# Kernel optimization log

Hardware: AMD Instinct MI355X
Metric: run time of the kernel (lower is better)

The kernel has to match this reference:

```python
import jax, jax.numpy as jnp
import numpy as np

EPS = 1e-5

def _conv3x3(x, w):
    # x: [n,c,h,w], w: [o,c,3,3], stride 1, padding 1 (SAME)
    return jax.lax.conv_general_dilated(x, w, (1, 1), 'SAME',
                                        dimension_numbers=('NCHW', 'OIHW', 'NCHW'))

def _bn(x, g, b, m, v):
    # inference-mode BatchNorm2d with running stats
    s = g / jnp.sqrt(v + EPS)
    return x * s[:, None, None] + (b - m * s)[:, None, None]

def _lrelu(x):
    return jnp.where(x > 0, x, 0.2 * x)

def _conv1x1(x, w, b):
    # w: [o,c] (1x1 conv kernel collapsed)
    return jnp.einsum('nchw,oc->nohw', x, w) + b[:, None, None]

def _conv_relu(x, w, g, b, m, v):
    return _lrelu(_bn(_conv3x3(x, w), g, b, m, v))

def _pam(f, Wq, bq, Wk, bk, Wv, bv, alpha):
    n, c, h, w = f.shape
    hw = h * w
    q = _conv1x1(f, Wq, bq).reshape(n, -1, hw)   # [n,cr,hw]
    k = _conv1x1(f, Wk, bk).reshape(n, -1, hw)   # [n,cr,hw]
    # attention[i,j] over spatial tokens, softmax along j
    attn = jax.nn.softmax(jnp.einsum('nci,ncj->nij', q, k), axis=-1)  # [n,hw,hw]
    v = _conv1x1(f, Wv, bv).reshape(n, c, hw)    # [n,c,hw]
    # torch: bmm(v, attn^T) -> out[:, :, i] = sum_j v[:, :, j] * attn[i, j]
    out = jnp.einsum('ncj,nij->nci', v, attn).reshape(n, c, h, w)
    return alpha * out + f

def _cam(f, W1, b1, W2, b2):
    s = jnp.mean(f, axis=(2, 3), keepdims=True)  # AdaptiveAvgPool2d(1)
    s = _lrelu(_conv1x1(s, W1, b1))
    s = jax.nn.sigmoid(_conv1x1(s, W2, b2))
    return f * s

def _upx2(x):
    n, c, h, w = x.shape
    return jax.image.resize(x, (n, c, 2 * h, 2 * w), 'bilinear')

def setup_inputs() -> dict:
    key = jax.random.key(0)
    ks = jax.random.split(key, 16)
    N, C, H, W_ = 4, 512, 64, 64
    CR, NC = C // 8, 64
    f32 = jnp.float32
    def nrm(k, shape, s=0.05):
        return jax.random.normal(k, shape, f32) * s
    return {
        'x': jax.random.normal(ks[0], (N, C, H, W_), f32),
        'W_pam_in': nrm(ks[1], (C, C, 3, 3)),
        'pam_gamma': jnp.ones((C,), f32), 'pam_beta': jnp.zeros((C,), f32),
        'pam_mean': nrm(ks[2], (C,)), 'pam_var': jax.random.uniform(ks[3], (C,), f32) + 0.5,
        'Wq': nrm(ks[4], (CR, C)), 'bq': jnp.zeros((CR,), f32),
        'Wk': nrm(ks[5], (CR, C)), 'bk': jnp.zeros((CR,), f32),
        'Wv': nrm(ks[6], (C, C)), 'bv': jnp.zeros((C,), f32),
        'alpha': nrm(ks[7], (1,), 1.0),
        'W_pam_out': nrm(ks[8], (NC, C)), 'b_pam_out': jnp.zeros((NC,), f32),
        'W_cam_in': nrm(ks[9], (C, C, 3, 3)),
        'cam_gamma': jnp.ones((C,), f32), 'cam_beta': jnp.zeros((C,), f32),
        'cam_mean': nrm(ks[10], (C,)), 'cam_var': jax.random.uniform(ks[11], (C,), f32) + 0.5,
        'Wc1': nrm(ks[12], (CR, C)), 'bc1': jnp.zeros((CR,), f32),
        'Wc2': nrm(ks[13], (C, CR)), 'bc2': jnp.zeros((C,), f32),
        'W_cam_out': nrm(ks[14], (NC, C)), 'b_cam_out': jnp.zeros((NC,), f32),
    }

def reference(x, W_pam_in, pam_gamma, pam_beta, pam_mean, pam_var,
              Wq, bq, Wk, bk, Wv, bv, alpha, W_pam_out, b_pam_out,
              W_cam_in, cam_gamma, cam_beta, cam_mean, cam_var,
              Wc1, bc1, Wc2, bc2, W_cam_out, b_cam_out):
    pam_feat = _conv_relu(x, W_pam_in, pam_gamma, pam_beta, pam_mean, pam_var)
    pam_feat = _pam(pam_feat, Wq, bq, Wk, bk, Wv, bv, alpha)
    pam_feat = _upx2(_conv1x1(pam_feat, W_pam_out, b_pam_out))
    cam_feat = _conv_relu(x, W_cam_in, cam_gamma, cam_beta, cam_mean, cam_var)
    cam_feat = _cam(cam_feat, Wc1, bc1, Wc2, bc2)
    cam_feat = _upx2(_conv1x1(cam_feat, W_cam_out, b_cam_out))
    return pam_feat + cam_feat
```

## Files before the change

### kernel.cpp

```cpp
#include <hip/hip_runtime.h>
#include <hip/hip_bf16.h>
#include <math.h>

#define N_  4
#define C_  512
#define H_  64
#define W_  64
#define HW_ 4096
#define CR_ 64
#define NC_ 64
#define EPSV 1e-5f

typedef __attribute__((ext_vector_type(8))) __bf16 bf16x8;
typedef __attribute__((ext_vector_type(4))) float f32x4;
typedef __hip_bfloat16 bf16s;

__device__ __forceinline__ unsigned short bfb(float f) {
    union { bf16s h; unsigned short u; } cv;
    cv.h = __float2bfloat16(f);
    return cv.u;
}

__device__ __forceinline__ int swz8(int row, int ch) {
    return row * 64 + ((ch ^ (row & 7)) << 3);
}

__global__ __launch_bounds__(256) void k_xpose(
    const float* __restrict__ x, bf16s* __restrict__ xbT)
{
    __shared__ float xs[64][65];
    const int tid = threadIdx.x;
    const int n = blockIdx.z, c0 = blockIdx.y * 64, p0 = blockIdx.x * 64;
    for (int e = tid; e < 4096; e += 256) {
        int ci = e >> 6, pi = e & 63;
        xs[ci][pi] = x[((size_t)(n*C_ + c0 + ci))*HW_ + p0 + pi];
    }
    __syncthreads();
    for (int e = tid; e < 4096; e += 256) {
        int pi = e >> 6, ci = e & 63;
        xbT[((size_t)n*HW_ + p0 + pi)*C_ + c0 + ci] = __float2bfloat16(xs[ci][pi]);
    }
}

__global__ __launch_bounds__(256) void k_wprep(
    const float* __restrict__ w, bf16s* __restrict__ wb)
{
    int e = blockIdx.x * 256 + threadIdx.x;
    int c = e & 511; int r = e >> 9;
    int tap = r % 9; int o = r / 9;
    wb[e] = __float2bfloat16(w[((size_t)o*C_ + c)*9 + tap]);
}

__global__ __launch_bounds__(256) void k_wcast(
    const float* __restrict__ in, bf16s* __restrict__ out, int nElem)
{
    int e = blockIdx.x * 256 + threadIdx.x;
    if (e < nElem) out[e] = __float2bfloat16(in[e]);
}

__global__ __launch_bounds__(256, 2) void k_conv3x3_mfma(
    const bf16s* __restrict__ xbT, const bf16s* __restrict__ wb,
    const float* __restrict__ gamma, const float* __restrict__ beta,
    const float* __restrict__ mean, const float* __restrict__ var,
    float* __restrict__ out, bf16s* __restrict__ featT,
    float* __restrict__ csum, int mode)
{
    __shared__ bf16s aL[3][128][40];
    __shared__ bf16s bL[132][40];
    const int tid = threadIdx.x;
    const int n  = blockIdx.z;
    const int o0 = blockIdx.y * 128;
    const int pt = blockIdx.x;
    const int y0 = pt * 2;
    const int lane = tid & 63;
    const int wid  = tid >> 6;
    const int wr = wid >> 1, wc = wid & 1;
    const int lr = lane & 15, cb = lane >> 4;

    const int ao  = tid >> 2;
    const int ac  = (tid & 3) * 8;
    const int t0  = tid >> 2;
    const int t1  = t0 + 64;
    const int t2  = t0 + 128;
    const int ry1 = t1 >= 66 ? 1 : 0;
    const int xi1 = t1 - (ry1 ? 66 : 0);

    f32x4 acc[4][4];
#pragma unroll
    for (int i = 0; i < 4; ++i)
#pragma unroll
        for (int j = 0; j < 4; ++j) acc[i][j] = (f32x4){0.f,0.f,0.f,0.f};

    int4 pA0, pA1, pA2, pA3, pA4, pA5, pB0, pB1, pB2;

#define CONV_AADDR(DXI, OHALF, C0, DYI) \
    (const int4*)(wb + ((size_t)(o0 + (OHALF) + ao)*9 + (DYI)*3 + (DXI))*C_ + (C0) + ac)

#define CONV_BLOAD(DST, RY, XI, C0, DYI, VALID)                               \
    {                                                                         \
        int row_ = y0 + (DYI) - 1 + (RY);                                     \
        int xc_  = (XI) - 1;                                                  \
        int4 v_ = {0,0,0,0};                                                  \
        if ((VALID) && row_ >= 0 && row_ < H_ && xc_ >= 0 && xc_ < W_)        \
            v_ = *(const int4*)(xbT +                                         \
                ((size_t)n*HW_ + row_*W_ + xc_)*C_ + (C0) + ac);              \
        DST = v_;                                                             \
    }

#define CONV_ISSUE(C0, DYI)                                                   \
    {                                                                         \
        pA0 = *CONV_AADDR(0,  0, C0, DYI);                                    \
        pA1 = *CONV_AADDR(0, 64, C0, DYI);                                    \
        pA2 = *CONV_AADDR(1,  0, C0, DYI);                                    \
        pA3 = *CONV_AADDR(1, 64, C0, DYI);                                    \
        pA4 = *CONV_AADDR(2,  0, C0, DYI);                                    \
        pA5 = *CONV_AADDR(2, 64, C0, DYI);                                    \
        CONV_BLOAD(pB0, 0, t0, C0, DYI, 1)                                    \
        CONV_BLOAD(pB1, ry1, xi1, C0, DYI, 1)                                 \
        CONV_BLOAD(pB2, 1, t2 - 66, C0, DYI, tid < 16)                        \
    }

    CONV_ISSUE(0, 0)
    int c0 = 0, dyi = 0;
    for (int it = 0; it < 48; ++it) {
        *(int4*)&aL[0][ao][ac]      = pA0;
        *(int4*)&aL[0][64 + ao][ac] = pA1;
        *(int4*)&aL[1][ao][ac]      = pA2;
        *(int4*)&aL[1][64 + ao][ac] = pA3;
        *(int4*)&aL[2][ao][ac]      = pA4;
        *(int4*)&aL[2][64 + ao][ac] = pA5;
        *(int4*)&bL[t0][ac] = pB0;
        *(int4*)&bL[t1][ac] = pB1;
        if (tid < 16) *(int4*)&bL[t2][ac] = pB2;
        __syncthreads();
        int nd = dyi + 1, nc = c0;
        if (nd == 3) { nd = 0; nc += 32; }
        if (it < 47) CONV_ISSUE(nc, nd)
#pragma unroll
        for (int dxi = 0; dxi < 3; ++dxi) {
            bf16x8 af[4], bfv[4];
#pragma unroll
            for (int fm = 0; fm < 4; ++fm)
                af[fm] = *(const bf16x8*)&aL[dxi][wr*64 + fm*16 + lr][cb*8];
#pragma unroll
            for (int fn = 0; fn < 4; ++fn) {
                int pg = wc*64 + fn*16 + lr;
                int ry = pg >> 6, xc = pg & 63;
                bfv[fn] = *(const bf16x8*)&bL[ry*66 + xc + dxi][cb*8];
            }
#pragma unroll
            for (int fm = 0; fm < 4; ++fm)
#pragma unroll
                for (int fn = 0; fn < 4; ++fn)
                    acc[fm][fn] = __builtin_amdgcn_mfma_f32_16x16x32_bf16(
                        af[fm], bfv[fn], acc[fm][fn], 0, 0, 0);
        }
        __syncthreads();
        c0 = nc; dyi = nd;
    }
#undef CONV_ISSUE
#undef CONV_BLOAD
#undef CONV_AADDR
#pragma unroll
    for (int fm = 0; fm < 4; ++fm) {
        float sc[4], sh[4];
        const int obase = o0 + wr*64 + fm*16 + cb*4;
#pragma unroll
        for (int r = 0; r < 4; ++r) {
            int o = obase + r;
            sc[r] = gamma[o] * rsqrtf(var[o] + EPSV);
            sh[r] = beta[o] - mean[o]*sc[r];
        }
        float ps[4] = {0.f, 0.f, 0.f, 0.f};
#pragma unroll
        for (int fn = 0; fn < 4; ++fn) {
            int pg = wc*64 + fn*16 + lr;
            int p  = pt*128 + pg;
            float vv[4];
#pragma unroll
            for (int r = 0; r < 4; ++r) {
                float t = fmaf(acc[fm][fn][r], sc[r], sh[r]);
                vv[r] = t > 0.f ? t : 0.2f*t;
                if (mode == 0)
                    out[((size_t)(n*C_ + obase + r))*HW_ + p] = vv[r];
                else
                    ps[r] += vv[r];
            }
            uint2 u;
            u.x = (unsigned)bfb(vv[0]) | ((unsigned)bfb(vv[1]) << 16);
            u.y = (unsigned)bfb(vv[2]) | ((unsigned)bfb(vv[3]) << 16);
            *(uint2*)&featT[((size_t)n*HW_ + p)*C_ + obase] = u;
        }
        if (mode != 0) {
#pragma unroll
            for (int r = 0; r < 4; ++r) {
                float s = ps[r];
                s += __shfl_xor(s, 1);
                s += __shfl_xor(s, 2);
                s += __shfl_xor(s, 4);
                s += __shfl_xor(s, 8);
                if (lr == 0) atomicAdd(&csum[n*C_ + obase + r], s);
            }
        }
    }
}

__global__ __launch_bounds__(256, 2) void k_gemm(
    const bf16s* __restrict__ A, const bf16s* __restrict__ Bt,
    const float* __restrict__ bias, const float* __restrict__ scale,
    void* __restrict__ outp, int O, int mode)
{
    __shared__ bf16s aL[64][40];
    __shared__ bf16s bL[256][40];
    const int tid = threadIdx.x;
    const int n  = blockIdx.z;
    const int p0 = blockIdx.x * 256;
    const int o0 = blockIdx.y * 64;
    const int lane = tid & 63;
    const int wid  = tid >> 6;
    const int lr = lane & 15, cb = lane >> 4;
    const int arow = tid >> 2, ach = (tid & 3) * 8;

    f32x4 acc[4][4];
#pragma unroll
    for (int i = 0; i < 4; ++i)
#pragma unroll
        for (int j = 0; j < 4; ++j) acc[i][j] = (f32x4){0.f,0.f,0.f,0.f};

    int4 pA, pB0, pB1, pB2, pB3;
    float4 pS0, pS1;

#define GEMM_ISSUE(C0)                                                        \
    {                                                                         \
        pA = *(const int4*)&A[(size_t)(o0 + arow)*C_ + (C0) + ach];           \
        if (scale) {                                                          \
            pS0 = *(const float4*)&scale[(size_t)n*C_ + (C0) + ach];          \
            pS1 = *(const float4*)&scale[(size_t)n*C_ + (C0) + ach + 4];      \
        }                                                                     \
        pB0 = *(const int4*)&Bt[((size_t)n*HW_ + p0 + arow      )*C_ + (C0) + ach]; \
        pB1 = *(const int4*)&Bt[((size_t)n*HW_ + p0 + arow +  64)*C_ + (C0) + ach]; \
        pB2 = *(const int4*)&Bt[((size_t)n*HW_ + p0 + arow + 128)*C_ + (C0) + ach]; \
        pB3 = *(const int4*)&Bt[((size_t)n*HW_ + p0 + arow + 192)*C_ + (C0) + ach]; \
    }

    GEMM_ISSUE(0)
    for (int c0 = 0; c0 < C_; c0 += 32) {
        if (scale) {
            const bf16s* sp = (const bf16s*)&pA;
            bf16s tmp[8];
            tmp[0] = __float2bfloat16(__bfloat162float(sp[0]) * pS0.x);
            tmp[1] = __float2bfloat16(__bfloat162float(sp[1]) * pS0.y);
            tmp[2] = __float2bfloat16(__bfloat162float(sp[2]) * pS0.z);
            tmp[3] = __float2bfloat16(__bfloat162float(sp[3]) * pS0.w);
            tmp[4] = __float2bfloat16(__bfloat162float(sp[4]) * pS1.x);
            tmp[5] = __float2bfloat16(__bfloat162float(sp[5]) * pS1.y);
            tmp[6] = __float2bfloat16(__bfloat162float(sp[6]) * pS1.z);
            tmp[7] = __float2bfloat16(__bfloat162float(sp[7]) * pS1.w);
            *(int4*)&aL[arow][ach] = *(int4*)tmp;
        } else {
            *(int4*)&aL[arow][ach] = pA;
        }
        *(int4*)&bL[arow      ][ach] = pB0;
        *(int4*)&bL[arow +  64][ach] = pB1;
        *(int4*)&bL[arow + 128][ach] = pB2;
        *(int4*)&bL[arow + 192][ach] = pB3;
        __syncthreads();
        if (c0 + 32 < C_) GEMM_ISSUE(c0 + 32)
        bf16x8 af[4], bfv[4];
#pragma unroll
        for (int fo = 0; fo < 4; ++fo)
            af[fo] = *(const bf16x8*)&aL[fo*16 + lr][cb*8];
#pragma unroll
        for (int fp = 0; fp < 4; ++fp)
            bfv[fp] = *(const bf16x8*)&bL[wid*64 + fp*16 + lr][cb*8];
#pragma unroll
        for (int fo = 0; fo < 4; ++fo)
#pragma unroll
            for (int fp = 0; fp < 4; ++fp)
                acc[fo][fp] = __builtin_amdgcn_mfma_f32_16x16x32_bf16(
                    af[fo], bfv[fp], acc[fo][fp], 0, 0, 0);
        __syncthreads();
    }
#undef GEMM_ISSUE
#pragma unroll
    for (int fo = 0; fo < 4; ++fo) {
        const int obase = o0 + fo*16 + cb*4;
        float bv[4];
#pragma unroll
        for (int r = 0; r < 4; ++r) bv[r] = bias[obase + r];
#pragma unroll
        for (int fp = 0; fp < 4; ++fp) {
            int p = p0 + wid*64 + fp*16 + lr;
            float v[4];
#pragma unroll
            for (int r = 0; r < 4; ++r) v[r] = acc[fo][fp][r] + bv[r];
            if (mode == 1) {
                uint2 u;
                u.x = (unsigned)bfb(v[0]) | ((unsigned)bfb(v[1]) << 16);
                u.y = (unsigned)bfb(v[2]) | ((unsigned)bfb(v[3]) << 16);
                *(uint2*)&((bf16s*)outp)[((size_t)n*HW_ + p)*O + (obase - o0)] = u;
            } else if (mode == 2) {
#pragma unroll
                for (int r = 0; r < 4; ++r)
                    ((bf16s*)outp)[((size_t)(n*O + obase + r))*HW_ + p] =
                        __float2bfloat16(v[r]);
            } else {
#pragma unroll
                for (int r = 0; r < 4; ++r)
                    ((float*)outp)[((size_t)(n*O + obase + r))*HW_ + p] = v[r];
            }
        }
    }
}

__global__ __launch_bounds__(256) void k_rowstats_mfma(
    const bf16s* __restrict__ qb, const bf16s* __restrict__ kb,
    float* __restrict__ rowm, float* __restrict__ rowl)
{
    __shared__ bf16s qs[4096];
    __shared__ bf16s ks[4096];
    const int tid = threadIdx.x;
    const int lid = blockIdx.x + (blockIdx.y << 6) + (blockIdx.z << 8);
    const int n  = lid & 3;
    const int jz = (lid >> 2) & 1;
    const int i0 = (lid >> 3) << 6;
    const int lane = tid & 63;
    const int wid  = tid >> 6;
    const int lr = lane & 15, cb = lane >> 4;

    for (int e = tid; e < 512; e += 256) {
        int row = e >> 3, ch = e & 7;
        *(int4*)&qs[swz8(row, ch)] =
            *(const int4*)&qb[((size_t)n*HW_ + i0 + row)*CR_ + ch*8];
    }
    const int krow = tid >> 3, kch = tid & 7;
    const bf16s* kbase = kb + (size_t)n*HW_*CR_ + (size_t)jz*2048*CR_ + kch*8;
    int4 kreg0 = *(const int4*)(kbase + (size_t)krow*CR_);
    int4 kreg1 = *(const int4*)(kbase + (size_t)(krow + 32)*CR_);
    __syncthreads();
    bf16x8 bq[2];
#pragma unroll
    for (int kk = 0; kk < 2; ++kk)
        bq[kk] = *(const bf16x8*)&qs[swz8(wid*16 + lr, kk*4 + cb)];

    float m_t = -INFINITY, l_t = 0.f;
    for (int t = 0; t < 32; ++t) {
        __syncthreads();
        *(int4*)&ks[swz8(krow, kch)] = kreg0;
        *(int4*)&ks[swz8(krow + 32, kch)] = kreg1;
        if (t < 31) {
            kreg0 = *(const int4*)(kbase + (size_t)((t+1)*64 + krow)*CR_);
            kreg1 = *(const int4*)(kbase + (size_t)((t+1)*64 + krow + 32)*CR_);
        }
        __syncthreads();
        f32x4 sv[4];
#pragma unroll
        for (int fj = 0; fj < 4; ++fj) {
            f32x4 s = (f32x4){0.f,0.f,0.f,0.f};
#pragma unroll
            for (int kk = 0; kk < 2; ++kk) {
                bf16x8 ak = *(const bf16x8*)&ks[swz8(fj*16 + lr, kk*4 + cb)];
                s = __builtin_amdgcn_mfma_f32_16x16x32_bf16(ak, bq[kk], s, 0, 0, 0);
            }
            sv[fj] = s;
        }
        float mx = m_t;
#pragma unroll
        for (int fj = 0; fj < 4; ++fj)
#pragma unroll
            for (int r = 0; r < 4; ++r) mx = fmaxf(mx, sv[fj][r]);
        float sum = 0.f;
#pragma unroll
        for (int fj = 0; fj < 4; ++fj)
#pragma unroll
            for (int r = 0; r < 4; ++r) sum += __expf(sv[fj][r] - mx);
        l_t = l_t * __expf(m_t - mx) + sum;
        m_t = mx;
    }
#pragma unroll
    for (int mask = 16; mask <= 32; mask <<= 1) {
        float mo = __shfl_xor(m_t, mask);
        float lo = __shfl_xor(l_t, mask);
        float m2 = fmaxf(m_t, mo);
        l_t = l_t * __expf(m_t - m2) + lo * __expf(mo - m2);
        m_t = m2;
    }
    if (cb == 0) {
        rowm[((size_t)jz*N_ + n)*HW_ + i0 + wid*16 + lr] = m_t;
        rowl[((size_t)jz*N_ + n)*HW_ + i0 + wid*16 + lr] = l_t;
    }
}

__global__ __launch_bounds__(256, 4) void k_pv_mfma(
    const bf16s* __restrict__ qb, const bf16s* __restrict__ kb,
    const bf16s* __restrict__ vb, const float* __restrict__ rowm,
    const float* __restrict__ rowl, const float* __restrict__ alpha,
    const float* __restrict__ feat, bf16s* __restrict__ featT)
{
    __shared__ bf16s ks[4096];
    __shared__ bf16s qps[4096];
    const int tid = threadIdx.x;
    const int lid = blockIdx.x + (blockIdx.y << 6) + (blockIdx.z << 8);
    const int k8  = lid & 7;
    const int n   = k8 >> 1;
    const int cc0 = (((lid >> 3) & 1) * 2 + (k8 & 1)) << 7;
    const int i0  = (lid >> 4) << 6;
    const int lane = tid & 63;
    const int wid  = tid >> 6;
    const int lr = lane & 15, cb = lane >> 4;

    for (int e = tid; e < 512; e += 256) {
        int row = e >> 3, ch = e & 7;
        *(int4*)&qps[swz8(row, ch)] =
            *(const int4*)&qb[((size_t)n*HW_ + i0 + row)*CR_ + ch*8];
    }
    const int krow = tid >> 3, kch = tid & 7;
    const bf16s* kbase = kb + (size_t)n*HW_*CR_ + kch*8;
    int4 kreg0 = *(const int4*)(kbase + (size_t)krow*CR_);
    int4 kreg1 = *(const int4*)(kbase + (size_t)(krow + 32)*CR_);
    __syncthreads();
    bf16x8 bq[2];
#pragma unroll
    for (int kk = 0; kk < 2; ++kk)
        bq[kk] = *(const bf16x8*)&qps[swz8(wid*16 + lr, kk*4 + cb)];

    const size_t sidx = (size_t)n*HW_ + i0 + wid*16 + lr;
    const float m0 = rowm[sidx], m1 = rowm[sidx + (size_t)N_*HW_];
    const float l0 = rowl[sidx], l1 = rowl[sidx + (size_t)N_*HW_];
    const float mreg = fmaxf(m0, m1);
    const float rinv = 1.f / (l0*__expf(m0 - mreg) + l1*__expf(m1 - mreg));
    const float al = alpha[0];

    f32x4 acc[2][4];
#pragma unroll
    for (int i = 0; i < 2; ++i)
#pragma unroll
        for (int j = 0; j < 4; ++j) acc[i][j] = (f32x4){0.f,0.f,0.f,0.f};

    const bf16s* vbase = vb + ((size_t)(n*C_ + cc0 + wid*32))*HW_;

    for (int jt = 0; jt < 64; ++jt) {
        *(int4*)&ks[swz8(krow, kch)] = kreg0;
        *(int4*)&ks[swz8(krow + 32, kch)] = kreg1;
        if (jt < 63) {
            kreg0 = *(const int4*)(kbase + (size_t)((jt+1)*64 + krow)*CR_);
            kreg1 = *(const int4*)(kbase + (size_t)((jt+1)*64 + krow + 32)*CR_);
        }
        __syncthreads();
#pragma unroll
        for (int fj = 0; fj < 4; ++fj) {
            f32x4 s = (f32x4){0.f,0.f,0.f,0.f};
#pragma unroll
            for (int kk = 0; kk < 2; ++kk) {
                bf16x8 ak = *(const bf16x8*)&ks[swz8(fj*16 + lr, kk*4 + cb)];
                s = __builtin_amdgcn_mfma_f32_16x16x32_bf16(ak, bq[kk], s, 0, 0, 0);
            }
            unsigned short b[4];
#pragma unroll
            for (int r = 0; r < 4; ++r)
                b[r] = bfb(__expf(s[r] - mreg) * rinv);
            uint2 u;
            u.x = (unsigned)b[0] | ((unsigned)b[1] << 16);
            u.y = (unsigned)b[2] | ((unsigned)b[3] << 16);
            *(uint2*)&qps[swz8(wid*16 + lr, fj*2 + (cb >> 1)) + (cb & 1)*4] = u;
        }
        __syncthreads();
        const bf16s* vj = vbase + jt*64;
#pragma unroll
        for (int kk2 = 0; kk2 < 2; ++kk2) {
            bf16x8 vf[2], pa[4];
#pragma unroll
            for (int fc2 = 0; fc2 < 2; ++fc2)
                vf[fc2] = *(const bf16x8*)(vj + (size_t)(fc2*16 + lr)*HW_
                                              + kk2*32 + cb*8);
#pragma unroll
            for (int fi = 0; fi < 4; ++fi)
                pa[fi] = *(const bf16x8*)&qps[swz8(fi*16 + lr, kk2*4 + cb)];
#pragma unroll
            for (int fc2 = 0; fc2 < 2; ++fc2)
#pragma unroll
                for (int fi = 0; fi < 4; ++fi)
                    acc[fc2][fi] = __builtin_amdgcn_mfma_f32_16x16x32_bf16(
                        vf[fc2], pa[fi], acc[fc2][fi], 0, 0, 0);
        }
    }
#pragma unroll
    for (int fc2 = 0; fc2 < 2; ++fc2) {
        const int ccl = wid*32 + fc2*16 + cb*4;
#pragma unroll
        for (int fi = 0; fi < 4; ++fi) {
            const int p = i0 + fi*16 + lr;
            const float* fp = &feat[((size_t)(n*C_ + cc0 + ccl))*HW_ + p];
            float v0 = fmaf(al, acc[fc2][fi][0], fp[0]);
            float v1 = fmaf(al, acc[fc2][fi][1], fp[(size_t)HW_]);
            float v2 = fmaf(al, acc[fc2][fi][2], fp[(size_t)2*HW_]);
            float v3 = fmaf(al, acc[fc2][fi][3], fp[(size_t)3*HW_]);
            uint2 u;
            u.x = (unsigned)bfb(v0) | ((unsigned)bfb(v1) << 16);
            u.y = (unsigned)bfb(v2) | ((unsigned)bfb(v3) << 16);
            *(uint2*)&featT[((size_t)n*HW_ + p)*C_ + cc0 + ccl] = u;
        }
    }
}

__global__ __launch_bounds__(64) void k_cmlp(
    const float* __restrict__ s0, const float* __restrict__ Wc1,
    const float* __restrict__ bc1, const float* __restrict__ Wc2,
    const float* __restrict__ bc2, float* __restrict__ s2)
{
    const int n = blockIdx.x, tid = threadIdx.x;
    __shared__ float s1s[64];
    float a = 0.f;
    for (int c = 0; c < C_; ++c)
        a = fmaf(Wc1[(size_t)tid*C_ + c], s0[n*C_ + c] * (1.f/HW_), a);
    a += bc1[tid];
    a = a > 0.f ? a : 0.2f*a;
    s1s[tid] = a;
    __syncthreads();
    for (int c = tid; c < C_; c += 64) {
        float b = 0.f;
        for (int i = 0; i < CR_; ++i) b = fmaf(Wc2[(size_t)c*CR_ + i], s1s[i], b);
        b += bc2[c];
        s2[n*C_ + c] = 1.f / (1.f + __expf(-b));
    }
}

__global__ __launch_bounds__(256) void k_up(
    const float* __restrict__ pl, const float* __restrict__ cl,
    float* __restrict__ out)
{
    int idx = blockIdx.x * 256 + threadIdx.x;
    int ox = idx & 127; int rest = idx >> 7;
    int oy = rest & 127; rest >>= 7;
    int o  = rest & 63;  int n = rest >> 6;
    float fy = oy*0.5f - 0.25f;
    float fx = ox*0.5f - 0.25f;
    int y0 = (int)floorf(fy); float wy = fy - y0;
    int x0 = (int)floorf(fx); float wx = fx - x0;
    int y0c = y0 < 0 ? 0 : y0;      int y1c = y0+1 > 63 ? 63 : y0+1;
    int x0c = x0 < 0 ? 0 : x0;      int x1c = x0+1 > 63 ? 63 : x0+1;
    const float* a = pl + ((size_t)(n*NC_ + o))*HW_;
    const float* b = cl + ((size_t)(n*NC_ + o))*HW_;
    float v00 = a[y0c*64+x0c] + b[y0c*64+x0c];
    float v01 = a[y0c*64+x1c] + b[y0c*64+x1c];
    float v10 = a[y1c*64+x0c] + b[y1c*64+x0c];
    float v11 = a[y1c*64+x1c] + b[y1c*64+x1c];
    out[idx] = (1.f-wy)*((1.f-wx)*v00 + wx*v01) + wy*((1.f-wx)*v10 + wx*v11);
}

extern "C" void kernel_launch(void* const* d_in, const int* in_sizes, int n_in,
                              void* d_out, int out_size, void* d_ws, size_t ws_size,
                              hipStream_t stream)
{
    const float* x         = (const float*)d_in[0];
    const float* W_pam_in  = (const float*)d_in[1];
    const float* pam_g     = (const float*)d_in[2];
    const float* pam_b     = (const float*)d_in[3];
    const float* pam_m     = (const float*)d_in[4];
    const float* pam_v     = (const float*)d_in[5];
    const float* Wq        = (const float*)d_in[6];
    const float* bq        = (const float*)d_in[7];
    const float* Wk        = (const float*)d_in[8];
    const float* bk        = (const float*)d_in[9];
    const float* Wv        = (const float*)d_in[10];
    const float* bv        = (const float*)d_in[11];
    const float* alpha     = (const float*)d_in[12];
    const float* W_pam_out = (const float*)d_in[13];
    const float* b_pam_out = (const float*)d_in[14];
    const float* W_cam_in  = (const float*)d_in[15];
    const float* cam_g     = (const float*)d_in[16];
    const float* cam_b     = (const float*)d_in[17];
    const float* cam_m     = (const float*)d_in[18];
    const float* cam_v     = (const float*)d_in[19];
    const float* Wc1       = (const float*)d_in[20];
    const float* bc1       = (const float*)d_in[21];
    const float* Wc2       = (const float*)d_in[22];
    const float* bc2       = (const float*)d_in[23];
    const float* W_cam_out = (const float*)d_in[24];
    const float* b_cam_out = (const float*)d_in[25];

    float* feat    = (float*)d_ws;
    float* pam_low = feat    + 8388608;
    float* rowm    = pam_low + 1048576;
    float* rowl    = rowm    + 32768;
    float* s0      = rowl    + 32768;
    float* s2      = s0      + 2048;
    bf16s* xbT     = (bf16s*)(s2 + 2048);
    bf16s* featTb  = xbT + 8388608;
    bf16s* vb      = featTb + 8388608;
    bf16s* qb      = vb + 8388608;
    bf16s* kb      = qb + 1048576;
    bf16s* wbp     = kb + 1048576;
    bf16s* Wqb     = wbp + 2359296;
    bf16s* Wkb     = Wqb + 32768;
    bf16s* Wvb     = Wkb + 32768;
    bf16s* Wpob    = Wvb + 262144;
    bf16s* Wcob    = Wpob + 32768;
    float* cam_low = (float*)qb;

    dim3 b256(256);
    k_xpose<<<dim3(64,8,4), b256, 0, stream>>>(x, xbT);
    k_wcast<<<dim3(128), b256, 0, stream>>>(Wq, Wqb, 32768);
    k_wcast<<<dim3(128), b256, 0, stream>>>(Wk, Wkb, 32768);
    k_wcast<<<dim3(1024), b256, 0, stream>>>(Wv, Wvb, 262144);
    k_wcast<<<dim3(128), b256, 0, stream>>>(W_pam_out, Wpob, 32768);
    k_wcast<<<dim3(128), b256, 0, stream>>>(W_cam_out, Wcob, 32768);
    hipMemsetAsync(s0, 0, 2048*sizeof(float), stream);
    k_wprep<<<dim3(9216), b256, 0, stream>>>(W_pam_in, wbp);
    k_conv3x3_mfma<<<dim3(32,4,4), b256, 0, stream>>>(
        xbT, wbp, pam_g, pam_b, pam_m, pam_v, feat, featTb, nullptr, 0);
    k_gemm<<<dim3(16,1,4), b256, 0, stream>>>(Wqb, featTb, bq, nullptr, qb, 64, 1);
    k_gemm<<<dim3(16,1,4), b256, 0, stream>>>(Wkb, featTb, bk, nullptr, kb, 64, 1);
    k_gemm<<<dim3(16,8,4), b256, 0, stream>>>(Wvb, featTb, bv, nullptr, vb, 512, 2);
    k_rowstats_mfma<<<dim3(64,4,2), b256, 0, stream>>>(qb, kb, rowm, rowl);
    k_pv_mfma<<<dim3(64,4,4), b256, 0, stream>>>(
        qb, kb, vb, rowm, rowl, alpha, feat, featTb);
    k_gemm<<<dim3(16,1,4), b256, 0, stream>>>(
        Wpob, featTb, b_pam_out, nullptr, pam_low, 64, 0);
    k_wprep<<<dim3(9216), b256, 0, stream>>>(W_cam_in, wbp);
    k_conv3x3_mfma<<<dim3(32,4,4), b256, 0, stream>>>(
        xbT, wbp, cam_g, cam_b, cam_m, cam_v, feat, featTb, s0, 1);
    k_cmlp<<<dim3(4), dim3(64), 0, stream>>>(s0, Wc1, bc1, Wc2, bc2, s2);
    k_gemm<<<dim3(16,1,4), b256, 0, stream>>>(
        Wcob, featTb, b_cam_out, s2, cam_low, 64, 0);
    k_up<<<dim3(16384), b256, 0, stream>>>(pam_low, cam_low, (float*)d_out);
}
```

Baseline: 482.7 us.

## Double-buffer K and P tiles, halve PV channel tile, defer softmax normalization

The rowstats kernel double-buffers K tiles in shared memory, so one barrier per iteration replaces two. The PV kernel now handles 64 channels per block instead of 128 and launches twice as many blocks with a higher occupancy hint. It double-buffers the P tile so the PV MFMAs for tile j-1 are interleaved with the QK and exp for tile j, and uses setprio around the MFMAs. Softmax normalization by 1/l moves from each P element to a single scale of the accumulator in the epilogue, at the cost of recomputing QK^T twice as often across the grid.

```diff
diff --git a/kernel.cpp b/kernel.cpp
--- a/kernel.cpp
+++ b/kernel.cpp
@@ -318,7 +318,7 @@
     float* __restrict__ rowm, float* __restrict__ rowl)
 {
     __shared__ bf16s qs[4096];
-    __shared__ bf16s ks[4096];
+    __shared__ bf16s ks[2][4096];
     const int tid = threadIdx.x;
     const int lid = blockIdx.x + (blockIdx.y << 6) + (blockIdx.z << 8);
     const int n  = lid & 3;
@@ -337,6 +337,10 @@
     const bf16s* kbase = kb + (size_t)n*HW_*CR_ + (size_t)jz*2048*CR_ + kch*8;
     int4 kreg0 = *(const int4*)(kbase + (size_t)krow*CR_);
     int4 kreg1 = *(const int4*)(kbase + (size_t)(krow + 32)*CR_);
+    *(int4*)&ks[0][swz8(krow, kch)] = kreg0;
+    *(int4*)&ks[0][swz8(krow + 32, kch)] = kreg1;
+    kreg0 = *(const int4*)(kbase + (size_t)(64 + krow)*CR_);
+    kreg1 = *(const int4*)(kbase + (size_t)(64 + krow + 32)*CR_);
     __syncthreads();
     bf16x8 bq[2];
 #pragma unroll
@@ -345,25 +349,26 @@
 
     float m_t = -INFINITY, l_t = 0.f;
     for (int t = 0; t < 32; ++t) {
-        __syncthreads();
-        *(int4*)&ks[swz8(krow, kch)] = kreg0;
-        *(int4*)&ks[swz8(krow + 32, kch)] = kreg1;
-        if (t < 31) {
-            kreg0 = *(const int4*)(kbase + (size_t)((t+1)*64 + krow)*CR_);
-            kreg1 = *(const int4*)(kbase + (size_t)((t+1)*64 + krow + 32)*CR_);
-        }
-        __syncthreads();
+        const bf16s* kst = ks[t & 1];
         f32x4 sv[4];
 #pragma unroll
         for (int fj = 0; fj < 4; ++fj) {
             f32x4 s = (f32x4){0.f,0.f,0.f,0.f};
 #pragma unroll
             for (int kk = 0; kk < 2; ++kk) {
-                bf16x8 ak = *(const bf16x8*)&ks[swz8(fj*16 + lr, kk*4 + cb)];
+                bf16x8 ak = *(const bf16x8*)&kst[swz8(fj*16 + lr, kk*4 + cb)];
                 s = __builtin_amdgcn_mfma_f32_16x16x32_bf16(ak, bq[kk], s, 0, 0, 0);
             }
             sv[fj] = s;
         }
+        if (t < 31) {
+            *(int4*)&ks[(t + 1) & 1][swz8(krow, kch)] = kreg0;
+            *(int4*)&ks[(t + 1) & 1][swz8(krow + 32, kch)] = kreg1;
+            if (t < 30) {
+                kreg0 = *(const int4*)(kbase + (size_t)((t+2)*64 + krow)*CR_);
+                kreg1 = *(const int4*)(kbase + (size_t)((t+2)*64 + krow + 32)*CR_);
+            }
+        }
         float mx = m_t;
 #pragma unroll
         for (int fj = 0; fj < 4; ++fj)
@@ -376,6 +381,7 @@
             for (int r = 0; r < 4; ++r) sum += __expf(sv[fj][r] - mx);
         l_t = l_t * __expf(m_t - mx) + sum;
         m_t = mx;
+        __syncthreads();
     }
 #pragma unroll
     for (int mask = 16; mask <= 32; mask <<= 1) {
@@ -391,27 +397,27 @@
     }
 }
 
-__global__ __launch_bounds__(256, 4) void k_pv_mfma(
+__global__ __launch_bounds__(256, 5) void k_pv_mfma(
     const bf16s* __restrict__ qb, const bf16s* __restrict__ kb,
     const bf16s* __restrict__ vb, const float* __restrict__ rowm,
     const float* __restrict__ rowl, const float* __restrict__ alpha,
     const float* __restrict__ feat, bf16s* __restrict__ featT)
 {
     __shared__ bf16s ks[4096];
-    __shared__ bf16s qps[4096];
+    __shared__ bf16s ps[2][4096];
     const int tid = threadIdx.x;
-    const int lid = blockIdx.x + (blockIdx.y << 6) + (blockIdx.z << 8);
+    const int lid = blockIdx.x + (blockIdx.y << 6) + (blockIdx.z << 9);
     const int k8  = lid & 7;
     const int n   = k8 >> 1;
-    const int cc0 = (((lid >> 3) & 1) * 2 + (k8 & 1)) << 7;
-    const int i0  = (lid >> 4) << 6;
+    const int cc0 = (((k8 & 1) << 2) + ((lid >> 3) & 3)) << 6;
+    const int i0  = (lid >> 5) << 6;
     const int lane = tid & 63;
     const int wid  = tid >> 6;
     const int lr = lane & 15, cb = lane >> 4;
 
     for (int e = tid; e < 512; e += 256) {
         int row = e >> 3, ch = e & 7;
-        *(int4*)&qps[swz8(row, ch)] =
+        *(int4*)&ps[0][swz8(row, ch)] =
             *(const int4*)&qb[((size_t)n*HW_ + i0 + row)*CR_ + ch*8];
     }
     const int krow = tid >> 3, kch = tid & 7;
@@ -419,87 +425,119 @@
     int4 kreg0 = *(const int4*)(kbase + (size_t)krow*CR_);
     int4 kreg1 = *(const int4*)(kbase + (size_t)(krow + 32)*CR_);
     __syncthreads();
-    bf16x8 bq[2];
-#pragma unroll
-    for (int kk = 0; kk < 2; ++kk)
-        bq[kk] = *(const bf16x8*)&qps[swz8(wid*16 + lr, kk*4 + cb)];
+    bf16x8 bq0 = *(const bf16x8*)&ps[0][swz8(wid*16 + lr, cb)];
+    bf16x8 bq1 = *(const bf16x8*)&ps[0][swz8(wid*16 + lr, 4 + cb)];
 
     const size_t sidx = (size_t)n*HW_ + i0 + wid*16 + lr;
-    const float m0 = rowm[sidx], m1 = rowm[sidx + (size_t)N_*HW_];
-    const float l0 = rowl[sidx], l1 = rowl[sidx + (size_t)N_*HW_];
-    const float mreg = fmaxf(m0, m1);
-    const float rinv = 1.f / (l0*__expf(m0 - mreg) + l1*__expf(m1 - mreg));
+    const float mreg = fmaxf(rowm[sidx], rowm[sidx + (size_t)N_*HW_]);
     const float al = alpha[0];
-
-    f32x4 acc[2][4];
-#pragma unroll
-    for (int i = 0; i < 2; ++i)
-#pragma unroll
-        for (int j = 0; j < 4; ++j) acc[i][j] = (f32x4){0.f,0.f,0.f,0.f};
-
-    const bf16s* vbase = vb + ((size_t)(n*C_ + cc0 + wid*32))*HW_;
+    __syncthreads();
+
+    f32x4 acc[4];
+#pragma unroll
+    for (int j = 0; j < 4; ++j) acc[j] = (f32x4){0.f,0.f,0.f,0.f};
+
+    const bf16s* vbase = vb + ((size_t)(n*C_ + cc0 + wid*16 + lr))*HW_ + cb*8;
+    bf16x8 vc0, vc1;
 
     for (int jt = 0; jt < 64; ++jt) {
         *(int4*)&ks[swz8(krow, kch)] = kreg0;
         *(int4*)&ks[swz8(krow + 32, kch)] = kreg1;
+        __syncthreads();
+        if (jt > 0) {
+            const bf16s* pp = ps[(jt - 1) & 1];
+            bf16x8 pa0 = *(const bf16x8*)&pp[swz8(     lr, cb)];
+            bf16x8 pa1 = *(const bf16x8*)&pp[swz8(16 + lr, cb)];
+            bf16x8 pa2 = *(const bf16x8*)&pp[swz8(32 + lr, cb)];
+            bf16x8 pa3 = *(const bf16x8*)&pp[swz8(48 + lr, cb)];
+            bf16x8 pb0 = *(const bf16x8*)&pp[swz8(     lr, 4 + cb)];
+            bf16x8 pb1 = *(const bf16x8*)&pp[swz8(16 + lr, 4 + cb)];
+            bf16x8 pb2 = *(const bf16x8*)&pp[swz8(32 + lr, 4 + cb)];
+            bf16x8 pb3 = *(const bf16x8*)&pp[swz8(48 + lr, 4 + cb)];
+            __builtin_amdgcn_s_setprio(1);
+            acc[0] = __builtin_amdgcn_mfma_f32_16x16x32_bf16(vc0, pa0, acc[0], 0, 0, 0);
+            acc[1] = __builtin_amdgcn_mfma_f32_16x16x32_bf16(vc0, pa1, acc[1], 0, 0, 0);
+            acc[2] = __builtin_amdgcn_mfma_f32_16x16x32_bf16(vc0, pa2, acc[2], 0, 0, 0);
+            acc[3] = __builtin_amdgcn_mfma_f32_16x16x32_bf16(vc0, pa3, acc[3], 0, 0, 0);
+            acc[0] = __builtin_amdgcn_mfma_f32_16x16x32_bf16(vc1, pb0, acc[0], 0, 0, 0);
+            acc[1] = __builtin_amdgcn_mfma_f32_16x16x32_bf16(vc1, pb1, acc[1], 0, 0, 0);
+            acc[2] = __builtin_amdgcn_mfma_f32_16x16x32_bf16(vc1, pb2, acc[2], 0, 0, 0);
+            acc[3] = __builtin_amdgcn_mfma_f32_16x16x32_bf16(vc1, pb3, acc[3], 0, 0, 0);
+            __builtin_amdgcn_s_setprio(0);
+        }
+        {
+            const bf16s* vj = vbase + jt*64;
+            vc0 = *(const bf16x8*)(vj);
+            vc1 = *(const bf16x8*)(vj + 32);
+        }
+        {
+            bf16s* pst = ps[jt & 1];
+            f32x4 s;
+#define PV_STEXP(FJ)                                                          \
+            s = (f32x4){0.f,0.f,0.f,0.f};                                     \
+            s = __builtin_amdgcn_mfma_f32_16x16x32_bf16(                      \
+                *(const bf16x8*)&ks[swz8(FJ*16 + lr, cb)], bq0, s, 0, 0, 0);  \
+            s = __builtin_amdgcn_mfma_f32_16x16x32_bf16(                      \
+                *(const bf16x8*)&ks[swz8(FJ*16 + lr, 4 + cb)], bq1, s, 0, 0, 0); \
+            {                                                                 \
+                unsigned short b0 = bfb(__expf(s[0] - mreg));                 \
+                unsigned short b1 = bfb(__expf(s[1] - mreg));                 \
+                unsigned short b2 = bfb(__expf(s[2] - mreg));                 \
+                unsigned short b3 = bfb(__expf(s[3] - mreg));                 \
+                uint2 u;                                                      \
+                u.x = (unsigned)b0 | ((unsigned)b1 << 16);                    \
+                u.y = (unsigned)b2 | ((unsigned)b3 << 16);                    \
+                *(uint2*)&pst[swz8(wid*16 + lr, FJ*2 + (cb >> 1)) + (cb & 1)*4] = u; \
+            }
+            PV_STEXP(0)
+            PV_STEXP(1)
+            PV_STEXP(2)
+            PV_STEXP(3)
+#undef PV_STEXP
+        }
         if (jt < 63) {
             kreg0 = *(const int4*)(kbase + (size_t)((jt+1)*64 + krow)*CR_);
             kreg1 = *(const int4*)(kbase + (size_t)((jt+1)*64 + krow + 32)*CR_);
         }
         __syncthreads();
-#pragma unroll
-        for (int fj = 0; fj < 4; ++fj) {
-            f32x4 s = (f32x4){0.f,0.f,0.f,0.f};
-#pragma unroll
-            for (int kk = 0; kk < 2; ++kk) {
-                bf16x8 ak = *(const bf16x8*)&ks[swz8(fj*16 + lr, kk*4 + cb)];
-                s = __builtin_amdgcn_mfma_f32_16x16x32_bf16(ak, bq[kk], s, 0, 0, 0);
-            }
-            unsigned short b[4];
-#pragma unroll
-            for (int r = 0; r < 4; ++r)
-                b[r] = bfb(__expf(s[r] - mreg) * rinv);
-            uint2 u;
-            u.x = (unsigned)b[0] | ((unsigned)b[1] << 16);
-            u.y = (unsigned)b[2] | ((unsigned)b[3] << 16);
-            *(uint2*)&qps[swz8(wid*16 + lr, fj*2 + (cb >> 1)) + (cb & 1)*4] = u;
-        }
-        __syncthreads();
-        const bf16s* vj = vbase + jt*64;
-#pragma unroll
-        for (int kk2 = 0; kk2 < 2; ++kk2) {
-            bf16x8 vf[2], pa[4];
-#pragma unroll
-            for (int fc2 = 0; fc2 < 2; ++fc2)
-                vf[fc2] = *(const bf16x8*)(vj + (size_t)(fc2*16 + lr)*HW_
-                                              + kk2*32 + cb*8);
-#pragma unroll
-            for (int fi = 0; fi < 4; ++fi)
-                pa[fi] = *(const bf16x8*)&qps[swz8(fi*16 + lr, kk2*4 + cb)];
-#pragma unroll
-            for (int fc2 = 0; fc2 < 2; ++fc2)
-#pragma unroll
-                for (int fi = 0; fi < 4; ++fi)
-                    acc[fc2][fi] = __builtin_amdgcn_mfma_f32_16x16x32_bf16(
-                        vf[fc2], pa[fi], acc[fc2][fi], 0, 0, 0);
-        }
-    }
-#pragma unroll
-    for (int fc2 = 0; fc2 < 2; ++fc2) {
-        const int ccl = wid*32 + fc2*16 + cb*4;
-#pragma unroll
-        for (int fi = 0; fi < 4; ++fi) {
-            const int p = i0 + fi*16 + lr;
-            const float* fp = &feat[((size_t)(n*C_ + cc0 + ccl))*HW_ + p];
-            float v0 = fmaf(al, acc[fc2][fi][0], fp[0]);
-            float v1 = fmaf(al, acc[fc2][fi][1], fp[(size_t)HW_]);
-            float v2 = fmaf(al, acc[fc2][fi][2], fp[(size_t)2*HW_]);
-            float v3 = fmaf(al, acc[fc2][fi][3], fp[(size_t)3*HW_]);
-            uint2 u;
-            u.x = (unsigned)bfb(v0) | ((unsigned)bfb(v1) << 16);
-            u.y = (unsigned)bfb(v2) | ((unsigned)bfb(v3) << 16);
-            *(uint2*)&featT[((size_t)n*HW_ + p)*C_ + cc0 + ccl] = u;
-        }
+    }
+    {
+        const bf16s* pp = ps[1];
+        bf16x8 pa0 = *(const bf16x8*)&pp[swz8(     lr, cb)];
+        bf16x8 pa1 = *(const bf16x8*)&pp[swz8(16 + lr, cb)];
+        bf16x8 pa2 = *(const bf16x8*)&pp[swz8(32 + lr, cb)];
+        bf16x8 pa3 = *(const bf16x8*)&pp[swz8(48 + lr, cb)];
+        bf16x8 pb0 = *(const bf16x8*)&pp[swz8(     lr, 4 + cb)];
+        bf16x8 pb1 = *(const bf16x8*)&pp[swz8(16 + lr, 4 + cb)];
+        bf16x8 pb2 = *(const bf16x8*)&pp[swz8(32 + lr, 4 + cb)];
+        bf16x8 pb3 = *(const bf16x8*)&pp[swz8(48 + lr, 4 + cb)];
+        acc[0] = __builtin_amdgcn_mfma_f32_16x16x32_bf16(vc0, pa0, acc[0], 0, 0, 0);
+        acc[1] = __builtin_amdgcn_mfma_f32_16x16x32_bf16(vc0, pa1, acc[1], 0, 0, 0);
+        acc[2] = __builtin_amdgcn_mfma_f32_16x16x32_bf16(vc0, pa2, acc[2], 0, 0, 0);
+        acc[3] = __builtin_amdgcn_mfma_f32_16x16x32_bf16(vc0, pa3, acc[3], 0, 0, 0);
+        acc[0] = __builtin_amdgcn_mfma_f32_16x16x32_bf16(vc1, pb0, acc[0], 0, 0, 0);
+        acc[1] = __builtin_amdgcn_mfma_f32_16x16x32_bf16(vc1, pb1, acc[1], 0, 0, 0);
+        acc[2] = __builtin_amdgcn_mfma_f32_16x16x32_bf16(vc1, pb2, acc[2], 0, 0, 0);
+        acc[3] = __builtin_amdgcn_mfma_f32_16x16x32_bf16(vc1, pb3, acc[3], 0, 0, 0);
+    }
+    const int ccl = wid*16 + cb*4;
+#pragma unroll
+    for (int fi = 0; fi < 4; ++fi) {
+        const int p = i0 + fi*16 + lr;
+        const size_t ei = (size_t)n*HW_ + p;
+        const float em0 = rowm[ei], em1 = rowm[ei + (size_t)N_*HW_];
+        const float emx = fmaxf(em0, em1);
+        const float rv  = 1.f /
+            (rowl[ei]*__expf(em0 - emx) + rowl[ei + (size_t)N_*HW_]*__expf(em1 - emx));
+        const float* fp = &feat[((size_t)(n*C_ + cc0 + ccl))*HW_ + p];
+        float v0 = fmaf(al, acc[fi][0]*rv, fp[0]);
+        float v1 = fmaf(al, acc[fi][1]*rv, fp[(size_t)HW_]);
+        float v2 = fmaf(al, acc[fi][2]*rv, fp[(size_t)2*HW_]);
+        float v3 = fmaf(al, acc[fi][3]*rv, fp[(size_t)3*HW_]);
+        uint2 u;
+        u.x = (unsigned)bfb(v0) | ((unsigned)bfb(v1) << 16);
+        u.y = (unsigned)bfb(v2) | ((unsigned)bfb(v3) << 16);
+        *(uint2*)&featT[((size_t)n*HW_ + p)*C_ + cc0 + ccl] = u;
     }
 }
 
@@ -613,7 +651,7 @@
     k_gemm<<<dim3(16,1,4), b256, 0, stream>>>(Wkb, featTb, bk, nullptr, kb, 64, 1);
     k_gemm<<<dim3(16,8,4), b256, 0, stream>>>(Wvb, featTb, bv, nullptr, vb, 512, 2);
     k_rowstats_mfma<<<dim3(64,4,2), b256, 0, stream>>>(qb, kb, rowm, rowl);
-    k_pv_mfma<<<dim3(64,4,4), b256, 0, stream>>>(
+    k_pv_mfma<<<dim3(64,8,4), b256, 0, stream>>>(
         qb, kb, vb, rowm, rowl, alpha, feat, featTb);
     k_gemm<<<dim3(16,1,4), b256, 0, stream>>>(
         Wpob, featTb, b_pam_out, nullptr, pam_low, 64, 0);
```

Result: slower. 525.8 us (+8.9%).
